# Performance work log

Hardware: AMD Instinct MI355X
Metric: run time of the kernel (lower is better)

Reference implementation:

```python
import jax, jax.numpy as jnp
import numpy as np

HIDDEN = 1024
NUM_HEADS = 16
HEAD_DIM = HIDDEN // NUM_HEADS
BLOCK_SIZE = 2048
LN_EPS = 1e-12


def layer_norm(x, g, b, eps=LN_EPS):
    mu = jnp.mean(x, axis=-1, keepdims=True)
    var = jnp.mean(jnp.square(x - mu), axis=-1, keepdims=True)
    return (x - mu) * jax.lax.rsqrt(var + eps) * g + b


def setup_inputs() -> dict:
    key = jax.random.key(0)
    ks = jax.random.split(key, 10)
    B, S_CTX, S_Q = 4, 8192, 2048
    scale = 1.0 / np.sqrt(HIDDEN)
    inp = {
        "input_ids": jax.random.normal(ks[0], (B, S_CTX, HIDDEN), jnp.float32),
        "query_input": jax.random.normal(ks[1], (B, S_Q, HIDDEN), jnp.float32),
        "Wq": jax.random.normal(ks[2], (HIDDEN, HIDDEN), jnp.float32) * scale,
        "bq": jnp.zeros((HIDDEN,), jnp.float32),
        "Wk": jax.random.normal(ks[3], (HIDDEN, HIDDEN), jnp.float32) * scale,
        "bk": jnp.zeros((HIDDEN,), jnp.float32),
        "Wv": jax.random.normal(ks[4], (HIDDEN, HIDDEN), jnp.float32) * scale,
        "bv": jnp.zeros((HIDDEN,), jnp.float32),
        "ln_g": jnp.ones((HIDDEN,), jnp.float32),
        "ln_b": jnp.zeros((HIDDEN,), jnp.float32),
        "host_id": 2,
    }
    return inp


def reference(input_ids, query_input, Wq, bq, Wk, bk, Wv, bv, ln_g, ln_b, host_id):
    B = input_ids.shape[0]
    start = host_id * BLOCK_SIZE  # host_id is a static Python int
    # Phase 1: local context encoding (anchor_key is computed in the original
    # but never used downstream, so it does not affect the output)
    local_block = input_ids[:, start:start + BLOCK_SIZE]          # (B, Skv, H)
    local_h = layer_norm(local_block, ln_g, ln_b)
    k = (local_h @ Wk + bk).reshape(B, BLOCK_SIZE, NUM_HEADS, HEAD_DIM)
    v = (local_h @ Wv + bv).reshape(B, BLOCK_SIZE, NUM_HEADS, HEAD_DIM)
    # Phase 2: query encoding; dropout is identity (p=0 / eval mode)
    Sq = query_input.shape[1]
    q_h = layer_norm(query_input, ln_g, ln_b)
    q = (q_h @ Wq + bq).reshape(B, Sq, NUM_HEADS, HEAD_DIM)
    scores = jnp.einsum("bqhd,bkhd->bhqk", q, k) / np.sqrt(HEAD_DIM)
    probs = jax.nn.softmax(scores, axis=-1)                       # (B, H, Sq, Skv)
    ctx = jnp.einsum("bhqk,bkhd->bqhd", probs, v)
    return ctx.reshape(B, Sq, HIDDEN)
```

## Files before the change

### kernel.cpp

```cpp
#include <hip/hip_runtime.h>

#define B_    4
#define SCTX  8192
#define SQ    2048
#define SK    2048
#define HID   1024
#define NH    16
#define HD    64
#define MQ    (B_*SQ)
#define MK    (B_*SK)

typedef float f32x4  __attribute__((ext_vector_type(4)));
typedef short bf16x8 __attribute__((ext_vector_type(8)));

__device__ __forceinline__ unsigned short f2b(float f) {
    union { float f; unsigned u; } v; v.f = f;
    unsigned r = v.u + 0x7FFFu + ((v.u >> 16) & 1u);
    return (unsigned short)(r >> 16);
}

__device__ __forceinline__ unsigned short f2b_fast(float f) {
    union { float f; unsigned u; } v; v.f = f;
    return (unsigned short)((v.u + 0x8000u) >> 16);
}

__device__ __forceinline__ int decode_host_id(const unsigned* p) {
    unsigned w0 = p[0];
    int hid;
    if (w0 > 0u && w0 < 8u) hid = (int)w0;
    else if (w0 == 0u) {
        unsigned w1 = p[1];
        hid = (w1 == 0u) ? 0 : (int)__hiloint2double((int)w1, 0);
    } else hid = (int)__uint_as_float(w0);
    if (hid < 0) hid = 0;
    if (hid > SCTX/SK - 1) hid = SCTX/SK - 1;
    return hid;
}

__device__ __forceinline__ void gload16(const unsigned short* g, unsigned short* l) {
    __builtin_amdgcn_global_load_lds(
        (const __attribute__((address_space(1))) void*)g,
        (__attribute__((address_space(3))) void*)l, 16, 0, 0);
}

__global__ __launch_bounds__(256) void ln_tr_kernel(
        const float* __restrict__ query,
        const float* __restrict__ input_ids,
        const unsigned* __restrict__ host_id,
        const float* __restrict__ g,
        const float* __restrict__ lb,
        unsigned short* __restrict__ hq,
        unsigned short* __restrict__ hk,
        const float* __restrict__ Wq,
        const float* __restrict__ Wk,
        const float* __restrict__ Wv,
        unsigned short* __restrict__ Wtq,
        unsigned short* __restrict__ Wtk,
        unsigned short* __restrict__ Wtv) {
    __shared__ unsigned short tile[64][66];
    int bid = blockIdx.x;
    if (bid < 4096) {
        int lane = threadIdx.x & 63;
        int w = threadIdx.x >> 6;
        int row = bid * 4 + w;
        int start = decode_host_id(host_id) * SK;
        const float* src;
        unsigned short* dst;
        if (row < MQ) {
            src = query + (size_t)row * HID;
            dst = hq + (size_t)row * HID;
        } else {
            int r = row - MQ;
            int b = r >> 11, s = r & 2047;
            src = input_ids + ((size_t)b * SCTX + start + s) * HID;
            dst = hk + (size_t)r * HID;
        }
        float4 x[4];
        #pragma unroll
        for (int i = 0; i < 4; i++) x[i] = ((const float4*)src)[lane + i*64];
        float s1 = 0.0f, s2 = 0.0f;
        #pragma unroll
        for (int i = 0; i < 4; i++) {
            s1 += x[i].x + x[i].y + x[i].z + x[i].w;
            s2 += x[i].x*x[i].x + x[i].y*x[i].y + x[i].z*x[i].z + x[i].w*x[i].w;
        }
        #pragma unroll
        for (int off = 1; off < 64; off <<= 1) {
            s1 += __shfl_xor(s1, off, 64);
            s2 += __shfl_xor(s2, off, 64);
        }
        float mu   = s1 * (1.0f / HID);
        float var  = s2 * (1.0f / HID) - mu * mu;
        float rstd = rsqrtf(fmaxf(var, 0.0f) + 1e-12f);
        #pragma unroll
        for (int i = 0; i < 4; i++) {
            float4 gv = ((const float4*)g)[lane + i*64];
            float4 bv = ((const float4*)lb)[lane + i*64];
            ushort4 o;
            o.x = f2b((x[i].x - mu) * rstd * gv.x + bv.x);
            o.y = f2b((x[i].y - mu) * rstd * gv.y + bv.y);
            o.z = f2b((x[i].z - mu) * rstd * gv.z + bv.z);
            o.w = f2b((x[i].w - mu) * rstd * gv.w + bv.w);
            ((ushort4*)dst)[lane + i*64] = o;
        }
    } else {
        int id = bid - 4096;
        int z = id >> 8;
        int tid = id & 255;
        const float* src = (z == 0) ? Wq : (z == 1) ? Wk : Wv;
        unsigned short* dst = (z == 0) ? Wtq : (z == 1) ? Wtk : Wtv;
        int tx = threadIdx.x & 63;
        int ty = threadIdx.x >> 6;
        int k0 = (tid & 15) * 64;
        int n0 = (tid >> 4) * 64;
        for (int i = ty; i < 64; i += 4)
            tile[i][tx] = f2b(src[(size_t)(k0 + i) * HID + n0 + tx]);
        __syncthreads();
        for (int i = ty; i < 64; i += 4)
            dst[(size_t)(n0 + i) * HID + k0 + tx] = tile[tx][i];
    }
}

#define BM 128
#define BN 128
#define BKg 32

__global__ __launch_bounds__(256, 3) void gemm3_kernel(
        const unsigned short* __restrict__ hq,
        const unsigned short* __restrict__ hk,
        const unsigned short* __restrict__ Wtq,
        const unsigned short* __restrict__ Wtk,
        const unsigned short* __restrict__ Wtv,
        const float* __restrict__ bq,
        const float* __restrict__ bk,
        const float* __restrict__ bv,
        unsigned short* __restrict__ Qb,
        unsigned short* __restrict__ Kb,
        unsigned short* __restrict__ Vtb) {
    __shared__ __align__(16) unsigned short As[2][BM * BKg];
    __shared__ __align__(16) unsigned short Bs[2][BN * BKg];

    int z = blockIdx.z;
    const unsigned short* A  = (z == 0) ? hq : hk;
    const unsigned short* Bt = (z == 0) ? Wtq : (z == 1) ? Wtk : Wtv;
    const float* bias        = (z == 0) ? bq  : (z == 1) ? bk  : bv;
    unsigned short* out      = (z == 0) ? Qb  : (z == 1) ? Kb  : Vtb;
    float scale = (z == 0) ? 0.18033688f : 1.0f;
    int epi = (z == 2);

    int t = threadIdx.x;
    int lane = t & 63;
    int w = t >> 6;
    int wr = w >> 1, wc = w & 1;
    int qd = lane >> 4, c = lane & 15;

    int bid = (int)(blockIdx.y * gridDim.x + blockIdx.x);
    int xcd = bid & 7, kk = bid >> 3;
    int bx = xcd * 8 + (kk & 7);
    int by = kk >> 3;
    size_t m0 = (size_t)bx * BM;
    size_t n0 = (size_t)by * BN;

    int s0 = t, s1 = t + 256;
    int ar0 = s0 >> 2, ac0 = (s0 & 3) * 8;
    int ar1 = s1 >> 2, ac1 = (s1 & 3) * 8;

#define STAGE(buf, kk0) do { \
    gload16(A  + (m0 + ar0) * HID + (kk0) + ac0, &As[buf][s0 * 8]); \
    gload16(A  + (m0 + ar1) * HID + (kk0) + ac1, &As[buf][s1 * 8]); \
    gload16(Bt + (n0 + ar0) * HID + (kk0) + ac0, &Bs[buf][s0 * 8]); \
    gload16(Bt + (n0 + ar1) * HID + (kk0) + ac1, &Bs[buf][s1 * 8]); \
} while (0)

#define COMPUTE(buf) do { \
    bf16x8 a[4], b[4]; \
    _Pragma("unroll") \
    for (int mi = 0; mi < 4; mi++) \
        a[mi] = *(const bf16x8*)(&As[buf][(wr*64 + mi*16 + c) * BKg + qd*8]); \
    _Pragma("unroll") \
    for (int ni = 0; ni < 4; ni++) \
        b[ni] = *(const bf16x8*)(&Bs[buf][(wc*64 + ni*16 + c) * BKg + qd*8]); \
    _Pragma("unroll") \
    for (int mi = 0; mi < 4; mi++) \
        _Pragma("unroll") \
        for (int ni = 0; ni < 4; ni++) \
            acc[mi][ni] = __builtin_amdgcn_mfma_f32_16x16x32_bf16(a[mi], b[ni], acc[mi][ni], 0, 0, 0); \
} while (0)

    f32x4 acc[4][4] = {};
    STAGE(0, 0);
    int cur = 0;
    for (int kt = 0; kt < HID/BKg - 1; kt++) {
        STAGE(cur ^ 1, (kt + 1) * BKg);
        asm volatile("s_waitcnt vmcnt(4)" ::: "memory");
        __builtin_amdgcn_s_barrier();
        COMPUTE(cur);
        asm volatile("s_waitcnt lgkmcnt(0)" ::: "memory");
        __builtin_amdgcn_s_barrier();
        cur ^= 1;
    }
    asm volatile("s_waitcnt vmcnt(0)" ::: "memory");
    __builtin_amdgcn_s_barrier();
    COMPUTE(cur);
#undef STAGE
#undef COMPUTE

    #pragma unroll
    for (int ni = 0; ni < 4; ni++) {
        int n = (int)n0 + wc*64 + ni*16 + c;
        float bn = bias[n];
        #pragma unroll
        for (int mi = 0; mi < 4; mi++) {
            int mbase = (int)m0 + wr*64 + mi*16 + qd*4;
            if (epi == 0) {
                #pragma unroll
                for (int r = 0; r < 4; r++)
                    out[(size_t)(mbase + r) * HID + n] = f2b((acc[mi][ni][r] + bn) * scale);
            } else {
                int bb = mbase >> 11, s = mbase & 2047;
                int h = n >> 6, d = n & 63;
                ushort4 pk;
                pk.x = f2b(acc[mi][ni][0] + bn);
                pk.y = f2b(acc[mi][ni][1] + bn);
                pk.z = f2b(acc[mi][ni][2] + bn);
                pk.w = f2b(acc[mi][ni][3] + bn);
                *(ushort4*)(out + (((size_t)(bb*NH + h))*HD + d)*SK + s) = pk;
            }
        }
    }
}

__global__ __launch_bounds__(64) void attn_kernel(
        const unsigned short* __restrict__ Q,
        const unsigned short* __restrict__ K,
        const unsigned short* __restrict__ Vt,
        float* __restrict__ out) {
    __shared__ __align__(16) unsigned short P[64][72];
    int lane = threadIdx.x;
    int qd = lane >> 4, c = lane & 15;
    int q0 = blockIdx.x * 64;
    int h  = blockIdx.y;
    int b  = blockIdx.z;

    bf16x8 qf[4][2];
    #pragma unroll
    for (int mi = 0; mi < 4; mi++)
        #pragma unroll
        for (int ks = 0; ks < 2; ks++)
            qf[mi][ks] = *(const bf16x8*)(Q + ((size_t)(b*SQ + q0 + mi*16 + c))*HID + h*HD + ks*32 + qd*8);

    float lsum[4][4];
    f32x4 o[4][4] = {};
    #pragma unroll
    for (int mi = 0; mi < 4; mi++)
        #pragma unroll
        for (int r = 0; r < 4; r++) lsum[mi][r] = 0.0f;

    for (int kt = 0; kt < SK/64; kt++) {
        int key0 = kt * 64;
        bf16x8 kf[4][2];
        #pragma unroll
        for (int ni = 0; ni < 4; ni++)
            #pragma unroll
            for (int ks = 0; ks < 2; ks++)
                kf[ni][ks] = *(const bf16x8*)(K + ((size_t)(b*SK + key0 + ni*16 + c))*HID + h*HD + ks*32 + qd*8);
        f32x4 s[4][4] = {};
        #pragma unroll
        for (int mi = 0; mi < 4; mi++)
            #pragma unroll
            for (int ni = 0; ni < 4; ni++) {
                s[mi][ni] = __builtin_amdgcn_mfma_f32_16x16x32_bf16(qf[mi][0], kf[ni][0], s[mi][ni], 0, 0, 0);
                s[mi][ni] = __builtin_amdgcn_mfma_f32_16x16x32_bf16(qf[mi][1], kf[ni][1], s[mi][ni], 0, 0, 0);
            }
        bf16x8 vf[4][2];
        #pragma unroll
        for (int ni = 0; ni < 4; ni++)
            #pragma unroll
            for (int ks = 0; ks < 2; ks++)
                vf[ni][ks] = *(const bf16x8*)(Vt + (((size_t)(b*NH + h))*HD + ni*16 + c)*SK + key0 + ks*32 + qd*8);
        #pragma unroll
        for (int mi = 0; mi < 4; mi++) {
            #pragma unroll
            for (int ni = 0; ni < 4; ni++)
                #pragma unroll
                for (int r = 0; r < 4; r++) {
                    float p = __builtin_amdgcn_exp2f(s[mi][ni][r]);
                    s[mi][ni][r] = p;
                    lsum[mi][r] += p;
                }
            #pragma unroll
            for (int ni = 0; ni < 4; ni++)
                #pragma unroll
                for (int r = 0; r < 4; r++)
                    P[mi*16 + qd*4 + r][ni*16 + c] = f2b_fast(s[mi][ni][r]);
        }
        asm volatile("s_waitcnt lgkmcnt(0)" ::: "memory");
        bf16x8 pf[4][2];
        #pragma unroll
        for (int mi = 0; mi < 4; mi++)
            #pragma unroll
            for (int ks = 0; ks < 2; ks++)
                pf[mi][ks] = *(const bf16x8*)(&P[mi*16 + c][ks*32 + qd*8]);
        #pragma unroll
        for (int mi = 0; mi < 4; mi++)
            #pragma unroll
            for (int ni = 0; ni < 4; ni++) {
                o[mi][ni] = __builtin_amdgcn_mfma_f32_16x16x32_bf16(pf[mi][0], vf[ni][0], o[mi][ni], 0, 0, 0);
                o[mi][ni] = __builtin_amdgcn_mfma_f32_16x16x32_bf16(pf[mi][1], vf[ni][1], o[mi][ni], 0, 0, 0);
            }
    }
    #pragma unroll
    for (int mi = 0; mi < 4; mi++)
        #pragma unroll
        for (int r = 0; r < 4; r++) {
            float l = lsum[mi][r];
            for (int off = 1; off < 16; off <<= 1) l += __shfl_xor(l, off, 16);
            lsum[mi][r] = 1.0f / l;
        }
    #pragma unroll
    for (int mi = 0; mi < 4; mi++)
        #pragma unroll
        for (int ni = 0; ni < 4; ni++)
            #pragma unroll
            for (int r = 0; r < 4; r++) {
                int m = q0 + mi*16 + qd*4 + r;
                out[((size_t)(b*SQ + m))*HID + h*HD + ni*16 + c] = o[mi][ni][r] * lsum[mi][r];
            }
}

extern "C" void kernel_launch(void* const* d_in, const int* in_sizes, int n_in,
                              void* d_out, int out_size, void* d_ws, size_t ws_size,
                              hipStream_t stream) {
    const float *input_ids = nullptr, *query = nullptr;
    const float *Ws[3] = {nullptr, nullptr, nullptr};
    const float *bs[5] = {nullptr, nullptr, nullptr, nullptr, nullptr};
    const unsigned *hostid = nullptr;
    int wi = 0, bi = 0;
    for (int i = 0; i < n_in; i++) {
        long sz = in_sizes[i];
        if      (sz == 33554432) input_ids = (const float*)d_in[i];
        else if (sz == 8388608)  query     = (const float*)d_in[i];
        else if (sz == 1048576)  { if (wi < 3) Ws[wi++] = (const float*)d_in[i]; }
        else if (sz == 1024)     { if (bi < 5) bs[bi++] = (const float*)d_in[i]; }
        else if (sz == 1 || sz == 2) hostid = (const unsigned*)d_in[i];
    }
    if (n_in != 11 || !input_ids || !query || wi != 3 || bi != 5 || !hostid) {
        input_ids = (const float*)d_in[0];  query = (const float*)d_in[1];
        Ws[0] = (const float*)d_in[2]; bs[0] = (const float*)d_in[3];
        Ws[1] = (const float*)d_in[4]; bs[1] = (const float*)d_in[5];
        Ws[2] = (const float*)d_in[6]; bs[2] = (const float*)d_in[7];
        bs[3] = (const float*)d_in[8]; bs[4] = (const float*)d_in[9];
        hostid = (const unsigned*)d_in[10];
    }
    const float *Wq = Ws[0], *Wk = Ws[1], *Wv = Ws[2];
    const float *bq = bs[0], *bk = bs[1], *bv = bs[2], *ln_g = bs[3], *ln_b = bs[4];
    float* out = (float*)d_out;

    char* ws = (char*)d_ws;
    unsigned short* hq  = (unsigned short*)ws; ws += (size_t)MQ * HID * 2;
    unsigned short* hk  = (unsigned short*)ws; ws += (size_t)MK * HID * 2;
    unsigned short* Wtq = (unsigned short*)ws; ws += (size_t)HID * HID * 2;
    unsigned short* Wtk = (unsigned short*)ws; ws += (size_t)HID * HID * 2;
    unsigned short* Wtv = (unsigned short*)ws; ws += (size_t)HID * HID * 2;
    unsigned short* Qb  = (unsigned short*)ws; ws += (size_t)MQ * HID * 2;
    unsigned short* Kb  = (unsigned short*)ws; ws += (size_t)MK * HID * 2;
    unsigned short* Vtb = (unsigned short*)ws; ws += (size_t)MK * HID * 2;

    ln_tr_kernel<<<4096 + 768, 256, 0, stream>>>(
        query, input_ids, hostid, ln_g, ln_b, hq, hk,
        Wq, Wk, Wv, Wtq, Wtk, Wtv);
    gemm3_kernel<<<dim3(MQ/BM, HID/BN, 3), 256, 0, stream>>>(
        hq, hk, Wtq, Wtk, Wtv, bq, bk, bv, Qb, Kb, Vtb);
    attn_kernel<<<dim3(SQ/64, NH, B_), 64, 0, stream>>>(Qb, Kb, Vtb, out);
}
```

Baseline: 415.9 us.

## Software-pipeline attention loop: prefetch next K/V tile and overlap QK with PV

Restructures the attention inner loop so the next tile's K and V fragments are loaded from global memory while the current tile's PV MFMAs run. The QK^T and softmax for the next tile are computed after PV, with P held in a double-buffered LDS array. The aim is to hide global load latency in a single-wave block. In exchange, register pressure rises from the extra kf and vf2 fragment sets, which could lower occupancy or cause spills.

```diff
diff --git a/kernel.cpp b/kernel.cpp
--- a/kernel.cpp
+++ b/kernel.cpp
@@ -235,7 +235,7 @@
         const unsigned short* __restrict__ K,
         const unsigned short* __restrict__ Vt,
         float* __restrict__ out) {
-    __shared__ __align__(16) unsigned short P[64][72];
+    __shared__ __align__(16) unsigned short P[2][64][72];
     int lane = threadIdx.x;
     int qd = lane >> 4, c = lane & 15;
     int q0 = blockIdx.x * 64;
@@ -256,43 +256,60 @@
         #pragma unroll
         for (int r = 0; r < 4; r++) lsum[mi][r] = 0.0f;
 
+    bf16x8 kf[4][2], vf[4][2], vf2[4][2];
+
+#define LOADK(key0) do { \
+    _Pragma("unroll") \
+    for (int ni = 0; ni < 4; ni++) \
+        _Pragma("unroll") \
+        for (int ks = 0; ks < 2; ks++) \
+            kf[ni][ks] = *(const bf16x8*)(K + ((size_t)(b*SK + (key0) + ni*16 + c))*HID + h*HD + ks*32 + qd*8); \
+} while (0)
+
+#define LOADV(dst, key0) do { \
+    _Pragma("unroll") \
+    for (int ni = 0; ni < 4; ni++) \
+        _Pragma("unroll") \
+        for (int ks = 0; ks < 2; ks++) \
+            dst[ni][ks] = *(const bf16x8*)(Vt + (((size_t)(b*NH + h))*HD + ni*16 + c)*SK + (key0) + ks*32 + qd*8); \
+} while (0)
+
+#define QK_SM(buf) do { \
+    f32x4 s[4][4] = {}; \
+    _Pragma("unroll") \
+    for (int mi = 0; mi < 4; mi++) \
+        _Pragma("unroll") \
+        for (int ni = 0; ni < 4; ni++) { \
+            s[mi][ni] = __builtin_amdgcn_mfma_f32_16x16x32_bf16(qf[mi][0], kf[ni][0], s[mi][ni], 0, 0, 0); \
+            s[mi][ni] = __builtin_amdgcn_mfma_f32_16x16x32_bf16(qf[mi][1], kf[ni][1], s[mi][ni], 0, 0, 0); \
+        } \
+    _Pragma("unroll") \
+    for (int mi = 0; mi < 4; mi++) { \
+        _Pragma("unroll") \
+        for (int ni = 0; ni < 4; ni++) \
+            _Pragma("unroll") \
+            for (int r = 0; r < 4; r++) { \
+                float p = __builtin_amdgcn_exp2f(s[mi][ni][r]); \
+                s[mi][ni][r] = p; \
+                lsum[mi][r] += p; \
+            } \
+        _Pragma("unroll") \
+        for (int ni = 0; ni < 4; ni++) \
+            _Pragma("unroll") \
+            for (int r = 0; r < 4; r++) \
+                P[buf][mi*16 + qd*4 + r][ni*16 + c] = f2b_fast(s[mi][ni][r]); \
+    } \
+} while (0)
+
+    LOADK(0);
+    LOADV(vf, 0);
+    QK_SM(0);
+
     for (int kt = 0; kt < SK/64; kt++) {
-        int key0 = kt * 64;
-        bf16x8 kf[4][2];
-        #pragma unroll
-        for (int ni = 0; ni < 4; ni++)
-            #pragma unroll
-            for (int ks = 0; ks < 2; ks++)
-                kf[ni][ks] = *(const bf16x8*)(K + ((size_t)(b*SK + key0 + ni*16 + c))*HID + h*HD + ks*32 + qd*8);
-        f32x4 s[4][4] = {};
-        #pragma unroll
-        for (int mi = 0; mi < 4; mi++)
-            #pragma unroll
-            for (int ni = 0; ni < 4; ni++) {
-                s[mi][ni] = __builtin_amdgcn_mfma_f32_16x16x32_bf16(qf[mi][0], kf[ni][0], s[mi][ni], 0, 0, 0);
-                s[mi][ni] = __builtin_amdgcn_mfma_f32_16x16x32_bf16(qf[mi][1], kf[ni][1], s[mi][ni], 0, 0, 0);
-            }
-        bf16x8 vf[4][2];
-        #pragma unroll
-        for (int ni = 0; ni < 4; ni++)
-            #pragma unroll
-            for (int ks = 0; ks < 2; ks++)
-                vf[ni][ks] = *(const bf16x8*)(Vt + (((size_t)(b*NH + h))*HD + ni*16 + c)*SK + key0 + ks*32 + qd*8);
-        #pragma unroll
-        for (int mi = 0; mi < 4; mi++) {
-            #pragma unroll
-            for (int ni = 0; ni < 4; ni++)
-                #pragma unroll
-                for (int r = 0; r < 4; r++) {
-                    float p = __builtin_amdgcn_exp2f(s[mi][ni][r]);
-                    s[mi][ni][r] = p;
-                    lsum[mi][r] += p;
-                }
-            #pragma unroll
-            for (int ni = 0; ni < 4; ni++)
-                #pragma unroll
-                for (int r = 0; r < 4; r++)
-                    P[mi*16 + qd*4 + r][ni*16 + c] = f2b_fast(s[mi][ni][r]);
+        int nxt = kt + 1;
+        if (nxt < SK/64) {
+            LOADK(nxt * 64);
+            LOADV(vf2, nxt * 64);
         }
         asm volatile("s_waitcnt lgkmcnt(0)" ::: "memory");
         bf16x8 pf[4][2];
@@ -300,7 +317,7 @@
         for (int mi = 0; mi < 4; mi++)
             #pragma unroll
             for (int ks = 0; ks < 2; ks++)
-                pf[mi][ks] = *(const bf16x8*)(&P[mi*16 + c][ks*32 + qd*8]);
+                pf[mi][ks] = *(const bf16x8*)(&P[kt & 1][mi*16 + c][ks*32 + qd*8]);
         #pragma unroll
         for (int mi = 0; mi < 4; mi++)
             #pragma unroll
@@ -308,7 +325,19 @@
                 o[mi][ni] = __builtin_amdgcn_mfma_f32_16x16x32_bf16(pf[mi][0], vf[ni][0], o[mi][ni], 0, 0, 0);
                 o[mi][ni] = __builtin_amdgcn_mfma_f32_16x16x32_bf16(pf[mi][1], vf[ni][1], o[mi][ni], 0, 0, 0);
             }
-    }
+        if (nxt < SK/64) {
+            QK_SM(nxt & 1);
+            #pragma unroll
+            for (int ni = 0; ni < 4; ni++)
+                #pragma unroll
+                for (int ks = 0; ks < 2; ks++)
+                    vf[ni][ks] = vf2[ni][ks];
+        }
+    }
+#undef LOADK
+#undef LOADV
+#undef QK_SM
+
     #pragma unroll
     for (int mi = 0; mi < 4; mi++)
         #pragma unroll
```

Result: no change. 415.3 us (-0.1%).
